# Performance work log

Measured on AMD Instinct MI355X. Metric: run time of the kernel, lower is better.

Reference implementation:

```python
import jax, jax.numpy as jnp
import numpy as np

N = 100000      # nodes
E = 1600000     # edges (before self-loops)
DIM = 128       # input feature dim
H = 5           # attention heads
C = 10          # per-head output channels
G = 256         # graphs in batch
NEG_SLOPE = 0.2 # PyG GATConv default


def setup_inputs() -> dict:
    key = jax.random.key(0)
    ks = jax.random.split(key, 8)
    x = jax.random.normal(ks[0], (N, DIM), jnp.float32)
    edge_index = jax.random.randint(ks[1], (2, E), 0, N, dtype=jnp.int64)
    batch = jnp.sort(jax.random.randint(ks[2], (N,), 0, G, dtype=jnp.int64))
    W = jax.random.normal(ks[3], (DIM, H * C), jnp.float32) * 0.05
    att_src = jax.random.normal(ks[4], (H, C), jnp.float32) * 0.1
    att_dst = jax.random.normal(ks[5], (H, C), jnp.float32) * 0.1
    bias = jnp.zeros((H * C,), jnp.float32)
    lin_w = jax.random.normal(ks[6], (H * C, 1), jnp.float32) * 0.1
    lin_b = jnp.zeros((1,), jnp.float32)
    return {"x": x, "W": W, "att_src": att_src, "att_dst": att_dst,
            "bias": bias, "lin_w": lin_w, "lin_b": lin_b,
            "edge_index": edge_index, "batch": batch}


def reference(x, W, att_src, att_dst, bias, lin_w, lin_b, edge_index, batch):
    n = x.shape[0]
    # PyG GATConv adds self-loops by default
    loop = jnp.arange(n, dtype=edge_index.dtype)
    src = jnp.concatenate([edge_index[0], loop])  # message sources j
    dst = jnp.concatenate([edge_index[1], loop])  # message targets i

    xw = (x @ W).reshape(n, H, C)                       # [N,H,C]
    a_src = jnp.einsum('nhc,hc->nh', xw, att_src)       # [N,H]
    a_dst = jnp.einsum('nhc,hc->nh', xw, att_dst)       # [N,H]

    logits = jax.nn.leaky_relu(a_src[src] + a_dst[dst], NEG_SLOPE)  # [Etot,H]
    # segment softmax over incoming edges per target node
    m = jax.ops.segment_max(logits, dst, num_segments=n)
    ex = jnp.exp(logits - m[dst])
    denom = jax.ops.segment_sum(ex, dst, num_segments=n)
    alpha = ex / denom[dst]                              # [Etot,H]

    msg = alpha[:, :, None] * xw[src]                    # [Etot,H,C]
    out = jax.ops.segment_sum(msg, dst, num_segments=n).reshape(n, H * C) + bias
    out = jax.nn.elu(out)                                # [N,H*C]

    # global_mean_pool over graph ids
    gsum = jax.ops.segment_sum(out, batch, num_segments=G)
    cnt = jax.ops.segment_sum(jnp.ones((n,), out.dtype), batch, num_segments=G)
    h = gsum / jnp.maximum(cnt, 1.0)[:, None]            # [G,H*C]

    # dropout p=0.5 is identity at inference (training=False)
    y = jax.nn.sigmoid(h @ lin_w + lin_b)                # [G,1]
    return (h, y)
```

## Files before the change

### kernel.cpp

```cpp
#include <hip/hip_runtime.h>
#include <hip/hip_bf16.h>
#include <hip/hip_fp8.h>
#include <math.h>

#define DIM 128
#define H 5
#define C 10
#define HC 50
#define NG 256
#define NEG_SLOPE 0.2f
#define UNR 8
#define WP 136
#define LOG2E 1.4426950408889634f

#define BSH 6
#define NB 1563
#define SB_CAP 1344
#define B1_BLOCKS 391
#define B1_CHUNK 4096

#define BKN2 32
#define ROWS_LDS2 (BKN2 * 64)

typedef short short8 __attribute__((ext_vector_type(8)));
typedef float floatx4 __attribute__((ext_vector_type(4)));
typedef float floatx2 __attribute__((ext_vector_type(2)));

__device__ inline short f2bf(float f) {
  __hip_bfloat16 h = __float2bfloat16(f);
  return *reinterpret_cast<short*>(&h);
}
#if __has_builtin(__builtin_amdgcn_cvt_f32_fp8)
__device__ inline float fp8tof(int b) { return __builtin_amdgcn_cvt_f32_fp8(b, 0); }
#else
__device__ inline float fp8tof(int b) {
  __hip_fp8_e4m3 v;
  v.__x = (__hip_fp8_storage_t)b;
  return (float)v;
}
#endif
#if __has_builtin(__builtin_amdgcn_cvt_pk_f32_fp8)
__device__ inline floatx2 fp8pk2(int us) {
  return __builtin_amdgcn_cvt_pk_f32_fp8(us, false);
}
#else
__device__ inline floatx2 fp8pk2(int us) {
  floatx2 r;
  r.x = fp8tof(us & 0xff);
  r.y = fp8tof((us >> 8) & 0xff);
  return r;
}
#endif
#if __has_builtin(__builtin_amdgcn_exp2f)
__device__ inline float fexp2(float x) { return __builtin_amdgcn_exp2f(x); }
#else
__device__ inline float fexp2(float x) { return exp2f(x); }
#endif
#if __has_builtin(__builtin_amdgcn_cvt_pk_fp8_f32)
__device__ inline unsigned ftofp8pk(float a, float b) {
  return (unsigned)__builtin_amdgcn_cvt_pk_fp8_f32(a, b, 0, false);
}
__device__ inline unsigned char ftofp8(float f) {
  return (unsigned char)(ftofp8pk(f, f) & 0xff);
}
#else
__device__ inline unsigned char ftofp8(float f) {
  __hip_fp8_e4m3 v(f);
  return v.__x;
}
__device__ inline unsigned ftofp8pk(float a, float b) {
  return (unsigned)ftofp8(a) | ((unsigned)ftofp8(b) << 8);
}
#endif

__global__ void k_zero(int* __restrict__ g) {
  int t = blockIdx.x * blockDim.x + threadIdx.x;
  if (t < NB) g[t] = 0;
}

__global__ __launch_bounds__(256) void k_split(
    const int* __restrict__ src, const int* __restrict__ dst,
    int* __restrict__ gcur, int* __restrict__ seg,
    const float* __restrict__ W, const float* __restrict__ att_src,
    const float* __restrict__ att_dst, short* __restrict__ swt_g,
    unsigned char* __restrict__ recb, int E_, int n) {
  __shared__ int hist[NB], curs[NB], baser[NB];
  int tid = threadIdx.x;
  if (blockIdx.x == B1_BLOCKS) {
    if (tid < 64) recb[((size_t)n << 6) + tid] = (tid < HC) ? 0x00 : 0xFE;
    for (int idx = tid; idx < HC * 128; idx += 256) {
      int j = idx >> 7, k = idx & 127;
      swt_g[idx] = f2bf(W[k * HC + j]);
    }
    if (tid < 128) {
      float sv[H] = {0.f, 0.f, 0.f, 0.f, 0.f};
      float dv[H] = {0.f, 0.f, 0.f, 0.f, 0.f};
#pragma unroll
      for (int c = 0; c < HC; ++c) {
        float w = W[tid * HC + c];
        sv[c / C] += w * att_src[c];
        dv[c / C] += w * att_dst[c];
      }
#pragma unroll
      for (int h = 0; h < H; ++h) {
        swt_g[(HC + h) * 128 + tid] = f2bf(sv[h] * LOG2E);
        swt_g[(55 + h) * 128 + tid] = f2bf(dv[h] * LOG2E);
      }
    } else {
      int k = tid - 128;
      for (int j = 60; j < 64; ++j) swt_g[j * 128 + k] = 0;
    }
    return;
  }
  for (int i = tid; i < NB; i += 256) hist[i] = 0;
  __syncthreads();
  int e0 = blockIdx.x * B1_CHUNK;
  int dreg[16];
#pragma unroll
  for (int k = 0; k < 16; ++k) {
    int e = e0 + (k << 8) + tid;
    dreg[k] = (e < E_) ? dst[e] : -1;
    if (dreg[k] >= 0) atomicAdd(&hist[((unsigned)dreg[k]) >> BSH], 1);
  }
  __syncthreads();
  for (int i = tid; i < NB; i += 256) {
    baser[i] = hist[i] ? atomicAdd(&gcur[i], hist[i]) : 0;
    curs[i] = 0;
  }
  __syncthreads();
#pragma unroll
  for (int k = 0; k < 16; ++k) {
    if (dreg[k] >= 0) {
      int d = dreg[k];
      int s = ((unsigned)d) >> BSH;
      int pos = baser[s] + atomicAdd(&curs[s], 1);
      if (pos < SB_CAP)
        seg[(size_t)s * SB_CAP + pos] = (src[e0 + (k << 8) + tid] << 6) | (d & 63);
    }
  }
}

__global__ __launch_bounds__(256) void k_mfma(
    const float* __restrict__ x, const short* __restrict__ swt_g,
    unsigned char* __restrict__ recb, __hip_bfloat16* __restrict__ adst, int n) {
  __shared__ short swt[64 * WP];
  for (int idx = threadIdx.x; idx < 1024; idx += 256) {
    int row = idx >> 4;
    *(short8*)&swt[row * WP + (idx & 15) * 8] = *(const short8*)(swt_g + idx * 8);
  }
  __syncthreads();
  int wv = threadIdx.x >> 6, lane = threadIdx.x & 63;
  int tiles = (n + 15) >> 4;
  int tile = blockIdx.x * 4 + wv;
  if (tile >= tiles) return;
  int r = lane & 15, q = lane >> 4;
  int row = tile * 16 + r;
  const float* xr = x + (size_t)min(row, n - 1) * DIM + q * 8;
  floatx4 acc[4];
#pragma unroll
  for (int nt = 0; nt < 4; ++nt) acc[nt] = (floatx4){0.f, 0.f, 0.f, 0.f};
#pragma unroll
  for (int ks = 0; ks < 4; ++ks) {
    float4 a0 = *(const float4*)(xr + ks * 32);
    float4 a1 = *(const float4*)(xr + ks * 32 + 4);
    short8 af;
    af[0] = f2bf(a0.x); af[1] = f2bf(a0.y); af[2] = f2bf(a0.z); af[3] = f2bf(a0.w);
    af[4] = f2bf(a1.x); af[5] = f2bf(a1.y); af[6] = f2bf(a1.z); af[7] = f2bf(a1.w);
    const short* wb = &swt[r * WP + q * 8 + ks * 32];
    short8 b0 = *(const short8*)(wb);
    short8 b1 = *(const short8*)(wb + 16 * WP);
    short8 b2 = *(const short8*)(wb + 32 * WP);
    short8 b3 = *(const short8*)(wb + 48 * WP);
    acc[0] = __builtin_amdgcn_mfma_f32_16x16x32_bf16(af, b0, acc[0], 0, 0, 0);
    acc[1] = __builtin_amdgcn_mfma_f32_16x16x32_bf16(af, b1, acc[1], 0, 0, 0);
    acc[2] = __builtin_amdgcn_mfma_f32_16x16x32_bf16(af, b2, acc[2], 0, 0, 0);
    acc[3] = __builtin_amdgcn_mfma_f32_16x16x32_bf16(af, b3, acc[3], 0, 0, 0);
  }
#pragma unroll
  for (int reg = 0; reg < 4; ++reg) {
    int nrow = tile * 16 + q * 4 + reg;
    if (nrow >= n) continue;
    size_t base = (size_t)nrow << 6;
#pragma unroll
    for (int nt = 0; nt < 4; ++nt) {
      int col = nt * 16 + r;
      float v = acc[nt][reg];
      if (col < 50) {
        recb[base + col] = ftofp8(v);
      } else if (col < 55) {
        *(unsigned short*)(recb + base + 50 + 2 * (col - 50)) =
            (unsigned short)(ftofp8pk(v, v) & 0xffff);
      } else if (col < 60) {
        adst[(size_t)nrow * H + (col - 55)] = __float2bfloat16(v);
      }
    }
  }
}

__global__ __launch_bounds__(256) void k_bin_gat(
    const int* __restrict__ seg, const int* __restrict__ gcur,
    const unsigned char* __restrict__ recb, const __hip_bfloat16* __restrict__ adst,
    const float* __restrict__ bias, float* __restrict__ out_node, int n) {
  __shared__ int rows[ROWS_LDS2];
  __shared__ __align__(16) int wbuf[4][128];
  int tid = threadIdx.x;
  int blk = blockIdx.x;
  int b = blk >> 1;
  int half32 = blk & 1;
  int lo = (b << BSH) + (half32 << 5);
  int hi = min(lo + BKN2, n);
  for (int k = tid; k < ROWS_LDS2; k += 256) rows[k] = n;
  __syncthreads();
  int cnt = min(gcur[b], SB_CAP);
  for (int k = tid; k < cnt; k += 256) {
    int e = seg[(size_t)b * SB_CAP + k];
    int dl = e & 63;
    if ((dl >> 5) == half32) {
      int s = ((unsigned)e) >> 6;
      int base = (dl & 31) << 6;
      int off = s & 63;
      int old = atomicExch(&rows[base + off], s);
      int probes = 0;
      while (old != n && probes < 128) {
        off = (off + 1) & 63;
        old = atomicExch(&rows[base + off], old);
        ++probes;
      }
    }
  }
  __syncthreads();

  int w = tid >> 6, lane = tid & 63;
  int* wb = wbuf[w];
  int nn = hi - lo;
  int pairsN = (nn + 1) >> 1;
  int hl = lane & 31;
  int hf = lane >> 5;
  bool chl = hl < 25;
  int h = hl / 5;
  int bpidx = ((hf << 5) + 25 + h) << 2;
  unsigned rowoff = (unsigned)(hl << 1);
  int rbase = hf << 6;

  for (int pr = w; pr < pairsN; pr += 4) {
    int i0l = pr * 2;
    int i1l = min(i0l + 1, nn - 1);
    int i0 = lo + i0l, i1 = lo + i1l;
    int iown = hf ? i1 : i0;
    float adi = 0.f;
    if (chl) adi = __bfloat162float(adst[(size_t)iown * H + h]);

    int jraw0 = rows[(i0l << 6) | lane];
    int jraw1 = rows[(i1l << 6) | lane];
    ((int2*)wb)[lane] = make_int2(n, n);
    bool v0 = (unsigned)jraw0 < (unsigned)n;
    unsigned long long mk0 = __ballot(v0);
    int deg0 = __popcll(mk0);
    int bel0 = __popcll(mk0 & ((1ull << lane) - 1ull));
    if (v0) wb[bel0] = jraw0;
    bool v1 = (unsigned)jraw1 < (unsigned)n;
    unsigned long long mk1 = __ballot(v1);
    int deg1 = __popcll(mk1);
    int bel1 = __popcll(mk1 & ((1ull << lane) - 1ull));
    if (v1) wb[64 + bel1] = jraw1;
    int mx = max(deg0, deg1);

    float dpA, dpB = 0.f, a0A, a0B = 0.f, a1A, a1B = 0.f;
    {
      int us = *(const unsigned short*)(recb + (((size_t)(unsigned)iown << 6) | rowoff));
      int asv = __builtin_amdgcn_ds_bpermute(bpidx, us);
      float asi = fp8tof(asv);
      float z = asi + adi;
      z = fmaxf(z, NEG_SLOPE * z);
      float pw = fexp2(z);
      floatx2 f = fp8pk2(us);
      dpA = pw;
      a0A = pw * f.x;
      a1A = pw * f.y;
    }
    for (int s0 = 0; s0 < mx; s0 += UNR) {
      int2 jp[UNR / 2];
#pragma unroll
      for (int up = 0; up < UNR / 2; ++up)
        jp[up] = *(const int2*)&wb[rbase + s0 + up * 2];
#pragma unroll
      for (int u = 0; u < UNR; ++u) {
        unsigned j = (unsigned)((u & 1) ? jp[u >> 1].y : jp[u >> 1].x);
        int us = *(const unsigned short*)(recb + (((size_t)j << 6) | rowoff));
        int asv = __builtin_amdgcn_ds_bpermute(bpidx, us);
        float asi = fp8tof(asv);
        float z = asi + adi;
        z = fmaxf(z, NEG_SLOPE * z);
        float pw = fexp2(z);
        floatx2 f = fp8pk2(us);
        if (u & 1) {
          dpB += pw;
          a0B = fmaf(pw, f.x, a0B);
          a1B = fmaf(pw, f.y, a1B);
        } else {
          dpA += pw;
          a0A = fmaf(pw, f.x, a0A);
          a1A = fmaf(pw, f.y, a1A);
        }
      }
    }
    if (chl) {
      float dp = dpA + dpB;
      float a0 = a0A + a0B, a1 = a1A + a1B;
      int c0 = hl * 2;
      float o0 = a0 / dp + bias[c0];
      o0 = o0 > 0.f ? o0 : __expf(o0) - 1.f;
      float o1 = a1 / dp + bias[c0 + 1];
      o1 = o1 > 0.f ? o1 : __expf(o1) - 1.f;
      float2 st;
      st.x = o0;
      st.y = o1;
      *(float2*)(out_node + (size_t)iown * HC + c0) = st;
    }
  }
}

__global__ __launch_bounds__(1024) void k_pool(
    const float* __restrict__ out_node, const int* __restrict__ batch,
    const float* __restrict__ lin_w, const float* __restrict__ lin_b,
    float* __restrict__ out, int n) {
  __shared__ int sb[2];
  __shared__ float sacc[16][HC];
  int g = blockIdx.x;
  int t = threadIdx.x;
  if (t < 2) {
    int target = g + t, lo = 0, hi = n;
    while (lo < hi) {
      int mid = (lo + hi) >> 1;
      if (batch[mid] < target) lo = mid + 1; else hi = mid;
    }
    sb[t] = lo;
  }
  __syncthreads();
  int s = sb[0], e = sb[1];
  int w = t >> 6, lane = t & 63;
  float a = 0.f;
  if (lane < HC)
    for (int i = s + w; i < e; i += 16) a += out_node[(size_t)i * HC + lane];
  if (lane < HC) sacc[w][lane] = a;
  __syncthreads();
  if (t < HC) {
    float r0 = 0.f, r1 = 0.f, r2 = 0.f, r3 = 0.f;
#pragma unroll
    for (int k = 0; k < 4; ++k) {
      r0 += sacc[k][t];
      r1 += sacc[4 + k][t];
      r2 += sacc[8 + k][t];
      r3 += sacc[12 + k][t];
    }
    float hv = ((r0 + r1) + (r2 + r3)) / fmaxf((float)(e - s), 1.f);
    out[g * HC + t] = hv;
    sacc[0][t] = hv * lin_w[t];
  }
  __syncthreads();
  if (t == 0) {
    float p = 0.f;
    for (int c = 0; c < HC; ++c) p += sacc[0][c];
    out[NG * HC + g] = 1.f / (1.f + __expf(-(p + lin_b[0])));
  }
}

extern "C" void kernel_launch(void* const* d_in, const int* in_sizes, int n_in,
                              void* d_out, int out_size, void* d_ws, size_t ws_size,
                              hipStream_t stream) {
  const float* x       = (const float*)d_in[0];
  const float* W       = (const float*)d_in[1];
  const float* att_src = (const float*)d_in[2];
  const float* att_dst = (const float*)d_in[3];
  const float* bias    = (const float*)d_in[4];
  const float* lin_w   = (const float*)d_in[5];
  const float* lin_b   = (const float*)d_in[6];
  const int*   eidx    = (const int*)d_in[7];
  const int*   batch   = (const int*)d_in[8];

  int n  = in_sizes[0] / DIM;
  int E_ = in_sizes[7] / 2;
  const int* srcp = eidx;
  const int* dstp = eidx + E_;

  char* p = (char*)d_ws;
  float* out_node = (float*)p; p += (size_t)n * HC * sizeof(float);
  unsigned char* recb = (unsigned char*)p; p += (size_t)(n + 1) * 64;
  __hip_bfloat16* adst = (__hip_bfloat16*)p; p += (size_t)n * H * sizeof(__hip_bfloat16);
  p = (char*)(((uintptr_t)p + 255) & ~(uintptr_t)255);
  short* swt_g = (short*)p; p += 64 * 128 * sizeof(short);
  p = (char*)(((uintptr_t)p + 255) & ~(uintptr_t)255);
  int* gcur = (int*)p; p += NB * sizeof(int);
  p = (char*)(((uintptr_t)p + 255) & ~(uintptr_t)255);
  int* seg = (int*)p; p += (size_t)NB * SB_CAP * sizeof(int);

  float* out = (float*)d_out;

  int tiles = (n + 15) / 16;
  int mfma_blocks = (tiles + 3) / 4;
  int nbk2 = (n + BKN2 - 1) / BKN2;

  k_zero<<<2, 1024, 0, stream>>>(gcur);
  k_split<<<B1_BLOCKS + 1, 256, 0, stream>>>(
      srcp, dstp, gcur, seg, W, att_src, att_dst, swt_g, recb, E_, n);
  k_mfma<<<mfma_blocks, 256, 0, stream>>>(x, swt_g, recb, adst, n);
  k_bin_gat<<<nbk2, 256, 0, stream>>>(seg, gcur, recb, adst, bias, out_node, n);
  k_pool<<<NG, 1024, 0, stream>>>(out_node, batch, lin_w, lin_b, out, n);
}
```

Measured before the change: 199.0 us.

## Transpose MFMA output for packed fp8 stores, enlarge split chunks, split GAT launch

The MFMA operands are swapped so each lane holds consecutive output columns for one node, which lets the epilogue write packed 4-byte fp8 words instead of scattered single-byte stores. Lane shuffles move the att_src/att_dst columns into place. The edge-binning kernel now gives each block twice as many edges with half as many blocks, trading more registers for fewer blocks and fewer global atomics. The GAT kernel is also split into two launches, one per half-bucket, which adds a launch and may reduce scheduling conflicts or overlap.

```diff
diff --git a/kernel.cpp b/kernel.cpp
--- a/kernel.cpp
+++ b/kernel.cpp
@@ -16,8 +16,8 @@
 #define BSH 6
 #define NB 1563
 #define SB_CAP 1344
-#define B1_BLOCKS 391
-#define B1_CHUNK 4096
+#define B1_BLOCKS 196
+#define B1_CHUNK 8192
 
 #define BKN2 32
 #define ROWS_LDS2 (BKN2 * 64)
@@ -58,7 +58,7 @@
 #endif
 #if __has_builtin(__builtin_amdgcn_cvt_pk_fp8_f32)
 __device__ inline unsigned ftofp8pk(float a, float b) {
-  return (unsigned)__builtin_amdgcn_cvt_pk_fp8_f32(a, b, 0, false);
+  return (unsigned)__builtin_amdgcn_cvt_pk_fp8_f32(a, b, 0, false) & 0xffffu;
 }
 __device__ inline unsigned char ftofp8(float f) {
   return (unsigned char)(ftofp8pk(f, f) & 0xff);
@@ -115,9 +115,9 @@
   for (int i = tid; i < NB; i += 256) hist[i] = 0;
   __syncthreads();
   int e0 = blockIdx.x * B1_CHUNK;
-  int dreg[16];
-#pragma unroll
-  for (int k = 0; k < 16; ++k) {
+  int dreg[32];
+#pragma unroll
+  for (int k = 0; k < 32; ++k) {
     int e = e0 + (k << 8) + tid;
     dreg[k] = (e < E_) ? dst[e] : -1;
     if (dreg[k] >= 0) atomicAdd(&hist[((unsigned)dreg[k]) >> BSH], 1);
@@ -129,7 +129,7 @@
   }
   __syncthreads();
 #pragma unroll
-  for (int k = 0; k < 16; ++k) {
+  for (int k = 0; k < 32; ++k) {
     if (dreg[k] >= 0) {
       int d = dreg[k];
       int s = ((unsigned)d) >> BSH;
@@ -154,8 +154,8 @@
   int tile = blockIdx.x * 4 + wv;
   if (tile >= tiles) return;
   int r = lane & 15, q = lane >> 4;
-  int row = tile * 16 + r;
-  const float* xr = x + (size_t)min(row, n - 1) * DIM + q * 8;
+  int node = tile * 16 + r;
+  const float* xr = x + (size_t)min(node, n - 1) * DIM + q * 8;
   floatx4 acc[4];
 #pragma unroll
   for (int nt = 0; nt < 4; ++nt) acc[nt] = (floatx4){0.f, 0.f, 0.f, 0.f};
@@ -163,48 +163,57 @@
   for (int ks = 0; ks < 4; ++ks) {
     float4 a0 = *(const float4*)(xr + ks * 32);
     float4 a1 = *(const float4*)(xr + ks * 32 + 4);
-    short8 af;
-    af[0] = f2bf(a0.x); af[1] = f2bf(a0.y); af[2] = f2bf(a0.z); af[3] = f2bf(a0.w);
-    af[4] = f2bf(a1.x); af[5] = f2bf(a1.y); af[6] = f2bf(a1.z); af[7] = f2bf(a1.w);
+    short8 bx;
+    bx[0] = f2bf(a0.x); bx[1] = f2bf(a0.y); bx[2] = f2bf(a0.z); bx[3] = f2bf(a0.w);
+    bx[4] = f2bf(a1.x); bx[5] = f2bf(a1.y); bx[6] = f2bf(a1.z); bx[7] = f2bf(a1.w);
     const short* wb = &swt[r * WP + q * 8 + ks * 32];
-    short8 b0 = *(const short8*)(wb);
-    short8 b1 = *(const short8*)(wb + 16 * WP);
-    short8 b2 = *(const short8*)(wb + 32 * WP);
-    short8 b3 = *(const short8*)(wb + 48 * WP);
-    acc[0] = __builtin_amdgcn_mfma_f32_16x16x32_bf16(af, b0, acc[0], 0, 0, 0);
-    acc[1] = __builtin_amdgcn_mfma_f32_16x16x32_bf16(af, b1, acc[1], 0, 0, 0);
-    acc[2] = __builtin_amdgcn_mfma_f32_16x16x32_bf16(af, b2, acc[2], 0, 0, 0);
-    acc[3] = __builtin_amdgcn_mfma_f32_16x16x32_bf16(af, b3, acc[3], 0, 0, 0);
-  }
-#pragma unroll
-  for (int reg = 0; reg < 4; ++reg) {
-    int nrow = tile * 16 + q * 4 + reg;
-    if (nrow >= n) continue;
-    size_t base = (size_t)nrow << 6;
-#pragma unroll
-    for (int nt = 0; nt < 4; ++nt) {
-      int col = nt * 16 + r;
-      float v = acc[nt][reg];
-      if (col < 50) {
-        recb[base + col] = ftofp8(v);
-      } else if (col < 55) {
-        *(unsigned short*)(recb + base + 50 + 2 * (col - 50)) =
-            (unsigned short)(ftofp8pk(v, v) & 0xffff);
-      } else if (col < 60) {
-        adst[(size_t)nrow * H + (col - 55)] = __float2bfloat16(v);
-      }
-    }
+    short8 w0 = *(const short8*)(wb);
+    short8 w1 = *(const short8*)(wb + 16 * WP);
+    short8 w2 = *(const short8*)(wb + 32 * WP);
+    short8 w3 = *(const short8*)(wb + 48 * WP);
+    acc[0] = __builtin_amdgcn_mfma_f32_16x16x32_bf16(w0, bx, acc[0], 0, 0, 0);
+    acc[1] = __builtin_amdgcn_mfma_f32_16x16x32_bf16(w1, bx, acc[1], 0, 0, 0);
+    acc[2] = __builtin_amdgcn_mfma_f32_16x16x32_bf16(w2, bx, acc[2], 0, 0, 0);
+    acc[3] = __builtin_amdgcn_mfma_f32_16x16x32_bf16(w3, bx, acc[3], 0, 0, 0);
+  }
+  float xa = __shfl_up(acc[3][3], 16);
+  float xb = __shfl_up(acc[3][1], 16);
+  float xc = __shfl_up(acc[3][2], 16);
+  if (node < n) {
+    size_t base = (size_t)node << 6;
+#pragma unroll
+    for (int nt = 0; nt < 3; ++nt) {
+      unsigned d = ftofp8pk(acc[nt][0], acc[nt][1]) |
+                   (ftofp8pk(acc[nt][2], acc[nt][3]) << 16);
+      *(unsigned*)(recb + base + nt * 16 + (q << 2)) = d;
+    }
+    unsigned d;
+    if (q == 0) {
+      d = ftofp8pk(acc[3][0], acc[3][1]) | (ftofp8pk(acc[3][2], acc[3][2]) << 16);
+    } else if (q == 1) {
+      d = ftofp8pk(xa, xa) | (ftofp8pk(acc[3][0], acc[3][0]) << 16);
+      adst[(size_t)node * H + 0] = __float2bfloat16(acc[3][3]);
+    } else if (q == 2) {
+      d = ftofp8pk(xb, xb) | (ftofp8pk(xc, xc) << 16);
+      adst[(size_t)node * H + 1] = __float2bfloat16(acc[3][0]);
+      adst[(size_t)node * H + 2] = __float2bfloat16(acc[3][1]);
+      adst[(size_t)node * H + 3] = __float2bfloat16(acc[3][2]);
+      adst[(size_t)node * H + 4] = __float2bfloat16(acc[3][3]);
+    } else {
+      d = 0;
+    }
+    *(unsigned*)(recb + base + 48 + (q << 2)) = d;
   }
 }
 
 __global__ __launch_bounds__(256) void k_bin_gat(
     const int* __restrict__ seg, const int* __restrict__ gcur,
     const unsigned char* __restrict__ recb, const __hip_bfloat16* __restrict__ adst,
-    const float* __restrict__ bias, float* __restrict__ out_node, int n) {
+    const float* __restrict__ bias, float* __restrict__ out_node, int n, int par) {
   __shared__ int rows[ROWS_LDS2];
   __shared__ __align__(16) int wbuf[4][128];
   int tid = threadIdx.x;
-  int blk = blockIdx.x;
+  int blk = blockIdx.x * 2 + par;
   int b = blk >> 1;
   int half32 = blk & 1;
   int lo = (b << BSH) + (half32 << 5);
@@ -404,6 +413,9 @@
   k_split<<<B1_BLOCKS + 1, 256, 0, stream>>>(
       srcp, dstp, gcur, seg, W, att_src, att_dst, swt_g, recb, E_, n);
   k_mfma<<<mfma_blocks, 256, 0, stream>>>(x, swt_g, recb, adst, n);
-  k_bin_gat<<<nbk2, 256, 0, stream>>>(seg, gcur, recb, adst, bias, out_node, n);
+  k_bin_gat<<<(nbk2 + 1) / 2, 256, 0, stream>>>(
+      seg, gcur, recb, adst, bias, out_node, n, 0);
+  k_bin_gat<<<nbk2 / 2, 256, 0, stream>>>(
+      seg, gcur, recb, adst, bias, out_node, n, 1);
   k_pool<<<NG, 1024, 0, stream>>>(out_node, batch, lin_w, lin_b, out, n);
 }
```

New measurement: 206.3 us. 3.7% more time.
